# Kernel tuning notes

Measured on AMD Instinct MI355X. Metric: run time of the kernel, lower is better.

The kernel has to match this reference:

```python
import jax, jax.numpy as jnp
import numpy as np

N = 4096
D = 1024

def setup_inputs() -> dict:
    key = jax.random.key(0)
    k1, k2, k3, k4, k5, k6 = jax.random.split(key, 6)
    x_l = jax.random.normal(k1, (1, N, D), dtype=jnp.float32)
    x_r = jax.random.normal(k2, (1, N, D), dtype=jnp.float32)
    # mask encodes: (u,v) in legal_pairs AND locator[u,v] endpoints not in bucket
    mask = jax.random.randint(k3, (N, N), 0, 2) > 0
    # xavier_uniform for bilinear matrix
    limit = float(np.sqrt(6.0 / (D + D)))
    matrix = jax.random.uniform(k4, (D, D), dtype=jnp.float32, minval=-limit, maxval=limit)
    bias = jnp.zeros((1,), dtype=jnp.float32)
    wl = jax.random.normal(k5, (1, D), dtype=jnp.float32) * 0.02
    bl = jnp.zeros((1,), dtype=jnp.float32)
    wr = jax.random.normal(k6, (1, D), dtype=jnp.float32) * 0.02
    br = jnp.zeros((1,), dtype=jnp.float32)
    return {"x_l": x_l, "x_r": x_r, "mask": mask, "matrix": matrix,
            "bias": bias, "wl": wl, "bl": bl, "wr": wr, "br": br, "s_ind": 0}

def reference(x_l, x_r, mask, matrix, bias, wl, bl, wr, br, s_ind):
    # biaffine: x_l @ M @ x_r^T + bias  -> [1, n, n]
    xm = jnp.einsum('bnl,lr->bnr', x_l, matrix)
    x = jnp.einsum('bnr,bmr->bnm', xm, x_r) + bias[0]
    # linear terms: lin_l(x_l) -> [1,n,1]; lin_r(x_r)^T -> [1,1,n]
    lin_l = jnp.einsum('bnl,ol->bno', x_l, wl) + bl  # [1, n, 1]
    lin_r = jnp.einsum('bnr,or->bno', x_r, wr) + br  # [1, n, 1]
    x = x + lin_l + jnp.swapaxes(lin_r, 1, 2)
    x = jax.nn.relu(x)
    x = x[0]  # squeeze batch -> [n, n]
    # vectorized form of the legal_pairs / hypergraph-bucket scatter loop
    scores = jnp.where(mask, x, jnp.zeros((), dtype=x.dtype))
    return (scores, x)
```

## Files before the change

kernel.cpp:

```cpp
#include <hip/hip_runtime.h>
#include <stdint.h>
#include <stddef.h>

#define NTOK 4096
#define DDIM 1024

typedef __attribute__((ext_vector_type(4))) float f32x4;
typedef __attribute__((ext_vector_type(8))) short s16x8;
typedef __attribute__((ext_vector_type(4))) unsigned short u16x4;
typedef __attribute__((ext_vector_type(4))) int i32x4;

__device__ __forceinline__ unsigned short f2bf(float f) {
  union { float f; unsigned u; } v; v.f = f;
  unsigned u = v.u + 0x7fffu + ((v.u >> 16) & 1u);
  return (unsigned short)(u >> 16);
}

__device__ __forceinline__ void gload_lds16(const void* g, void* l) {
  __builtin_amdgcn_global_load_lds(
      (const __attribute__((address_space(1))) void*)g,
      (__attribute__((address_space(3))) void*)l, 16, 0, 0);
}

#define VMWAIT(N) asm volatile("s_waitcnt vmcnt(" #N ")" ::: "memory")

__global__ void convlin_k(const float* __restrict__ x, const float* __restrict__ w,
                          const float* __restrict__ b0, const float* __restrict__ b1,
                          unsigned short* __restrict__ xb, float* __restrict__ lin) {
  int wv = threadIdx.x >> 6, lane = threadIdx.x & 63;
  int row = blockIdx.x * 4 + wv;
  const f32x4* xr = (const f32x4*)(x + (size_t)row * DDIM);
  const f32x4* w4 = (const f32x4*)w;
  u16x4* xb4 = (u16x4*)(xb + (size_t)row * DDIM);
  float s = 0.f;
  for (int j = lane; j < DDIM / 4; j += 64) {
    f32x4 a = xr[j], c = w4[j];
    s += a[0] * c[0] + a[1] * c[1] + a[2] * c[2] + a[3] * c[3];
    u16x4 o;
    o[0] = f2bf(a[0]); o[1] = f2bf(a[1]); o[2] = f2bf(a[2]); o[3] = f2bf(a[3]);
    xb4[j] = o;
  }
#pragma unroll
  for (int off = 32; off; off >>= 1) s += __shfl_down(s, off);
  if (lane == 0) lin[row] = s + b0[0] + (b1 ? b1[0] : 0.f);
}

__global__ void transpose_bf16_k(const float* __restrict__ M,
                                 unsigned short* __restrict__ Mt) {
  __shared__ unsigned short tile[32][33];
  int tx = threadIdx.x, ty = threadIdx.y;
  int bx = blockIdx.x, by = blockIdx.y;
  int x = bx * 32 + tx;
  for (int i = ty; i < 32; i += 8)
    tile[i][tx] = f2bf(M[(size_t)(by * 32 + i) * DDIM + x]);
  __syncthreads();
  int ox = by * 32 + tx;
  for (int i = ty; i < 32; i += 8)
    Mt[(size_t)(bx * 32 + i) * DDIM + ox] = tile[tx][i];
}

__global__ void detect_mask_k(const unsigned char* __restrict__ m, int* __restrict__ flag) {
  __shared__ int f;
  if (threadIdx.x == 0) f = 0;
  __syncthreads();
  int any = 0;
  for (int i = threadIdx.x; i < 4096; i += 256)
    if ((i & 3) && m[i]) any = 1;
  if (any) atomicOr(&f, 1);
  __syncthreads();
  if (threadIdx.x == 0) *flag = f;
}

__launch_bounds__(512, 4)
__global__ void gemm1_k(const unsigned short* __restrict__ A,
                        const unsigned short* __restrict__ B,
                        unsigned short* __restrict__ Cb) {
  constexpr int BM = 64, BN = 128, K = DDIM;
  constexpr int MF = 2, NF = 2, AI = 1, BI = 2;
  __shared__ unsigned short As[2][BM][64];
  __shared__ unsigned short Bs[2][BN][64];

  const int lin = blockIdx.x;
  const int cpx = gridDim.x >> 3;
  const int swz = (lin & 7) * cpx + (lin >> 3);
  const int bi = swz >> 3, bj = swz & 7;

  const int tid = threadIdx.x;
  const int wid = tid >> 6, lane = tid & 63;
  const int wr2 = wid >> 2, wc2 = wid & 3;
  const int l15 = lane & 15, l16 = lane >> 4;
  const int xm = lane & 7;

  const int srow0 = tid >> 3;
  const int swslot = (tid & 7) ^ (srow0 & 7);
  const unsigned short* Ag = A + (size_t)(bi * BM + srow0) * K + swslot * 8;
  const unsigned short* Bg = B + (size_t)(bj * BN + srow0) * K + swslot * 8;

  f32x4 acc[MF][NF] = {};

#define STAGE_G1(BUF, K0)                                                    \
  {                                                                          \
    _Pragma("unroll") for (int j = 0; j < AI; ++j)                           \
        gload_lds16(Ag + (size_t)(j * 64) * K + (K0),                        \
                    &As[BUF][0][0] + j * 4096 + wid * 512);                  \
    _Pragma("unroll") for (int j = 0; j < BI; ++j)                           \
        gload_lds16(Bg + (size_t)(j * 64) * K + (K0),                        \
                    &Bs[BUF][0][0] + j * 4096 + wid * 512);                  \
  }

  STAGE_G1(0, 0)
  VMWAIT(0);
  __builtin_amdgcn_s_barrier();

  for (int t = 0; t < 16; ++t) {
    const int cur = t & 1, nxt = cur ^ 1;
    if (t < 15) STAGE_G1(nxt, (t + 1) * 64)
#pragma unroll
    for (int kk = 0; kk < 2; ++kk) {
      s16x8 Areg[MF], Breg[NF];
#pragma unroll
      for (int m = 0; m < MF; ++m)
        Areg[m] = *(const s16x8*)&As[cur][wr2 * 32 + m * 16 + l15]
                                     [(((kk << 2) | l16) ^ xm) << 3];
#pragma unroll
      for (int n = 0; n < NF; ++n)
        Breg[n] = *(const s16x8*)&Bs[cur][wc2 * 32 + n * 16 + l15]
                                     [(((kk << 2) | l16) ^ xm) << 3];
      __builtin_amdgcn_s_setprio(1);
#pragma unroll
      for (int m = 0; m < MF; ++m)
#pragma unroll
        for (int n = 0; n < NF; ++n)
          acc[m][n] = __builtin_amdgcn_mfma_f32_16x16x32_bf16(
              Areg[m], Breg[n], acc[m][n], 0, 0, 0);
      __builtin_amdgcn_s_setprio(0);
    }
    VMWAIT(0);
    __builtin_amdgcn_s_barrier();
  }
#undef STAGE_G1

#pragma unroll
  for (int m = 0; m < MF; ++m) {
    int row0 = bi * BM + wr2 * 32 + m * 16 + 4 * l16;
#pragma unroll
    for (int n = 0; n < NF; ++n) {
      int col = bj * BN + wc2 * 32 + n * 16 + l15;
#pragma unroll
      for (int r = 0; r < 4; ++r)
        Cb[(size_t)(row0 + r) * DDIM + col] = f2bf(acc[m][n][r]);
    }
  }
}

__launch_bounds__(256, 2)
__global__ void gemm2_k(const unsigned short* __restrict__ A,
                        const unsigned short* __restrict__ B,
                        const float* __restrict__ linl,
                        const float* __restrict__ linr,
                        const void* __restrict__ mask,
                        const int* __restrict__ mflag,
                        float* __restrict__ scores,
                        float* __restrict__ xout) {
  constexpr int K = DDIM;
  __shared__ __align__(16) unsigned short sAB[4 * 8192];
  unsigned short* sA = sAB;
  unsigned short* sB = sAB + 2 * 8192;

  const int lin = blockIdx.x;
  const int xcd = lin & 7, s = lin >> 3;
  const int p = (s >> 5) * 8 + xcd;
  const int w = s & 31;
  const int bi = (p >> 2) * 4 + (w >> 3);
  const int bj = (p & 3) * 8 + (w & 7);

  const int tid = threadIdx.x;
  const int wid = tid >> 6, lane = tid & 63;
  const int wr2 = wid >> 1, wc2 = wid & 1;
  const int l15 = lane & 15, l16 = lane >> 4;
  const int xm = lane & 7;

  const int srow0 = tid >> 3;
  const int swslot = (tid & 7) ^ (srow0 & 7);
  const unsigned short* Ag = A + (size_t)(bi * 128 + srow0) * K + swslot * 8;
  const unsigned short* Bg = B + (size_t)(bj * 128 + srow0) * K + swslot * 8;

  f32x4 acc[4][4] = {};

#define STG2(BUF, K0)                                                        \
  {                                                                          \
    _Pragma("unroll") for (int j = 0; j < 4; ++j) {                          \
      gload_lds16(Ag + (size_t)(j * 32) * K + (K0),                          \
                  sA + (BUF)*8192 + j * 2048 + wid * 512);                   \
      gload_lds16(Bg + (size_t)(j * 32) * K + (K0),                          \
                  sB + (BUF)*8192 + j * 2048 + wid * 512);                   \
    }                                                                        \
  }

  STG2(0, 0)
  VMWAIT(0);
  __builtin_amdgcn_s_barrier();

  for (int t = 0; t < 16; ++t) {
    const int cur = t & 1, nxt = cur ^ 1;
    if (t < 15) STG2(nxt, (t + 1) * 64)
#pragma unroll
    for (int kk = 0; kk < 2; ++kk) {
      s16x8 Areg[4], Breg[4];
#pragma unroll
      for (int m = 0; m < 4; ++m)
        Areg[m] = *(const s16x8*)(sA + cur * 8192 +
                                  (wr2 * 64 + m * 16 + l15) * 64 +
                                  ((((kk << 2) | l16) ^ xm) << 3));
#pragma unroll
      for (int n = 0; n < 4; ++n)
        Breg[n] = *(const s16x8*)(sB + cur * 8192 +
                                  (wc2 * 64 + n * 16 + l15) * 64 +
                                  ((((kk << 2) | l16) ^ xm) << 3));
      __builtin_amdgcn_s_setprio(1);
#pragma unroll
      for (int m = 0; m < 4; ++m)
#pragma unroll
        for (int n = 0; n < 4; ++n)
          acc[m][n] = __builtin_amdgcn_mfma_f32_16x16x32_bf16(
              Areg[m], Breg[n], acc[m][n], 0, 0, 0);
      __builtin_amdgcn_s_setprio(0);
    }
    VMWAIT(0);
    __builtin_amdgcn_s_barrier();
  }
#undef STG2

  __syncthreads();
  float* Cf = (float*)sAB;
#pragma unroll
  for (int m = 0; m < 4; ++m) {
#pragma unroll
    for (int n = 0; n < 4; ++n) {
      int lc = wc2 * 64 + n * 16 + l15;
#pragma unroll
      for (int r = 0; r < 4; ++r) {
        int lr = wr2 * 64 + m * 16 + l16 * 4 + r;
        Cf[lr * 128 + (lc ^ (((lr >> 2) & 1) << 4))] = acc[m][n][r];
      }
    }
  }
  __syncthreads();

  const int mf = *mflag;
#pragma unroll
  for (int it = 0; it < 16; ++it) {
    int fid = it * 256 + tid;
    int lr = fid >> 5, sl = fid & 31;
    int c0 = sl << 2;
    int cs = c0 ^ (((lr >> 2) & 1) << 4);
    f32x4 v4 = *(const f32x4*)&Cf[lr * 128 + cs];
    int row = bi * 128 + lr;
    int colb = bj * 128 + c0;
    float ll = linl[row];
    f32x4 rr = *(const f32x4*)&linr[colb];
    size_t idx = (size_t)row * NTOK + colb;
    f32x4 o, sc;
    if (mf) {
      unsigned m4 = *(const unsigned*)((const unsigned char*)mask + idx);
#pragma unroll
      for (int e = 0; e < 4; ++e) {
        float v = v4[e] + ll + rr[e];
        v = v > 0.f ? v : 0.f;
        o[e] = v; sc[e] = ((m4 >> (8 * e)) & 255u) ? v : 0.f;
      }
    } else {
      i32x4 m4 = *(const i32x4*)((const int*)mask + idx);
#pragma unroll
      for (int e = 0; e < 4; ++e) {
        float v = v4[e] + ll + rr[e];
        v = v > 0.f ? v : 0.f;
        o[e] = v; sc[e] = m4[e] ? v : 0.f;
      }
    }
    *(f32x4*)&xout[idx] = o;
    *(f32x4*)&scores[idx] = sc;
  }
}

extern "C" void kernel_launch(void* const* d_in, const int* in_sizes, int n_in,
                              void* d_out, int out_size, void* d_ws, size_t ws_size,
                              hipStream_t stream) {
  const float* x_l    = (const float*)d_in[0];
  const float* x_r    = (const float*)d_in[1];
  const void*  maskp  = (const void*)d_in[2];
  const float* matrix = (const float*)d_in[3];
  const float* bias   = (const float*)d_in[4];
  const float* wl     = (const float*)d_in[5];
  const float* bl     = (const float*)d_in[6];
  const float* wr     = (const float*)d_in[7];
  const float* br     = (const float*)d_in[8];

  unsigned short* XLb = (unsigned short*)d_ws;
  unsigned short* XRb = XLb + (size_t)NTOK * DDIM;
  unsigned short* XMb = XRb + (size_t)NTOK * DDIM;
  unsigned short* Mtb = XMb + (size_t)NTOK * DDIM;
  float* lin_l = (float*)(Mtb + (size_t)DDIM * DDIM);
  float* lin_r = lin_l + NTOK;
  int* mflag = (int*)(lin_r + NTOK);

  float* scores = (float*)d_out;
  float* xout = scores + (size_t)NTOK * NTOK;

  convlin_k<<<NTOK / 4, 256, 0, stream>>>(x_l, wl, bl, bias, XLb, lin_l);
  convlin_k<<<NTOK / 4, 256, 0, stream>>>(x_r, wr, br, nullptr, XRb, lin_r);
  transpose_bf16_k<<<dim3(32, 32), dim3(32, 8), 0, stream>>>(matrix, Mtb);
  detect_mask_k<<<1, 256, 0, stream>>>((const unsigned char*)maskp, mflag);

  gemm1_k<<<512, 512, 0, stream>>>(XLb, Mtb, XMb);

  gemm2_k<<<1024, 256, 0, stream>>>(XMb, XRb, lin_l, lin_r, maskp, mflag,
                                    scores, xout);
}
```

Measured before the change: 108.2 us.

## Restructure gemm2 to 8 waves, BK=32 tiles and half-tile epilogue staging

The second GEMM kernel goes from 256 to 512 threads per block and each wave now owns a 64x32 sub-tile. The K step shrinks from 64 to 32 with a matching smaller LDS double buffer and new swizzle. The epilogue stages the 128x128 result through LDS in two 64-row halves so it fits the smaller shared buffer. The aim is higher occupancy and more waves to hide latency, at the cost of twice as many barriers per K loop and lower MFMA work per LDS load.

New measurement: 127.5 us. +17.8%, slower.

```diff
diff --git a/kernel.cpp b/kernel.cpp
--- a/kernel.cpp
+++ b/kernel.cpp
@@ -153,7 +153,7 @@
   }
 }
 
-__launch_bounds__(256, 2)
+__launch_bounds__(512, 8)
 __global__ void gemm2_k(const unsigned short* __restrict__ A,
                         const unsigned short* __restrict__ B,
                         const float* __restrict__ linl,
@@ -163,9 +163,9 @@
                         float* __restrict__ scores,
                         float* __restrict__ xout) {
   constexpr int K = DDIM;
-  __shared__ __align__(16) unsigned short sAB[4 * 8192];
+  __shared__ __align__(16) unsigned short sAB[4 * 4096];
   unsigned short* sA = sAB;
-  unsigned short* sB = sAB + 2 * 8192;
+  unsigned short* sB = sAB + 2 * 4096;
 
   const int lin = blockIdx.x;
   const int xcd = lin & 7, s = lin >> 3;
@@ -176,52 +176,47 @@
 
   const int tid = threadIdx.x;
   const int wid = tid >> 6, lane = tid & 63;
-  const int wr2 = wid >> 1, wc2 = wid & 1;
+  const int wr2 = wid >> 2, wc2 = wid & 3;
   const int l15 = lane & 15, l16 = lane >> 4;
-  const int xm = lane & 7;
-
-  const int srow0 = tid >> 3;
-  const int swslot = (tid & 7) ^ (srow0 & 7);
+  const int xs = (l15 >> 1) & 3;
+
+  const int srow0 = tid >> 2;
+  const int swslot = (tid & 3) ^ ((srow0 >> 1) & 3);
   const unsigned short* Ag = A + (size_t)(bi * 128 + srow0) * K + swslot * 8;
   const unsigned short* Bg = B + (size_t)(bj * 128 + srow0) * K + swslot * 8;
 
-  f32x4 acc[4][4] = {};
+  f32x4 acc[4][2] = {};
 
 #define STG2(BUF, K0)                                                        \
   {                                                                          \
-    _Pragma("unroll") for (int j = 0; j < 4; ++j) {                          \
-      gload_lds16(Ag + (size_t)(j * 32) * K + (K0),                          \
-                  sA + (BUF)*8192 + j * 2048 + wid * 512);                   \
-      gload_lds16(Bg + (size_t)(j * 32) * K + (K0),                          \
-                  sB + (BUF)*8192 + j * 2048 + wid * 512);                   \
-    }                                                                        \
+    gload_lds16(Ag + (K0), sA + (BUF)*4096 + wid * 512);                     \
+    gload_lds16(Bg + (K0), sB + (BUF)*4096 + wid * 512);                     \
   }
 
   STG2(0, 0)
   VMWAIT(0);
   __builtin_amdgcn_s_barrier();
 
-  for (int t = 0; t < 16; ++t) {
+  for (int t = 0; t < 32; ++t) {
     const int cur = t & 1, nxt = cur ^ 1;
-    if (t < 15) STG2(nxt, (t + 1) * 64)
-#pragma unroll
-    for (int kk = 0; kk < 2; ++kk) {
-      s16x8 Areg[4], Breg[4];
+    if (t < 31) STG2(nxt, (t + 1) * 32)
+    {
+      const unsigned short* As0 = sA + cur * 4096;
+      const unsigned short* Bs0 = sB + cur * 4096;
+      s16x8 Areg[4], Breg[2];
 #pragma unroll
       for (int m = 0; m < 4; ++m)
-        Areg[m] = *(const s16x8*)(sA + cur * 8192 +
-                                  (wr2 * 64 + m * 16 + l15) * 64 +
-                                  ((((kk << 2) | l16) ^ xm) << 3));
-#pragma unroll
-      for (int n = 0; n < 4; ++n)
-        Breg[n] = *(const s16x8*)(sB + cur * 8192 +
-                                  (wc2 * 64 + n * 16 + l15) * 64 +
-                                  ((((kk << 2) | l16) ^ xm) << 3));
+        Areg[m] = *(const s16x8*)(As0 + (wr2 * 64 + m * 16 + l15) * 32 +
+                                  ((l16 ^ xs) << 3));
+#pragma unroll
+      for (int n = 0; n < 2; ++n)
+        Breg[n] = *(const s16x8*)(Bs0 + (wc2 * 32 + n * 16 + l15) * 32 +
+                                  ((l16 ^ xs) << 3));
       __builtin_amdgcn_s_setprio(1);
 #pragma unroll
       for (int m = 0; m < 4; ++m)
 #pragma unroll
-        for (int n = 0; n < 4; ++n)
+        for (int n = 0; n < 2; ++n)
           acc[m][n] = __builtin_amdgcn_mfma_f32_16x16x32_bf16(
               Areg[m], Breg[n], acc[m][n], 0, 0, 0);
       __builtin_amdgcn_s_setprio(0);
@@ -231,55 +226,59 @@
   }
 #undef STG2
 
-  __syncthreads();
+  const int mf = *mflag;
   float* Cf = (float*)sAB;
 #pragma unroll
-  for (int m = 0; m < 4; ++m) {
-#pragma unroll
-    for (int n = 0; n < 4; ++n) {
-      int lc = wc2 * 64 + n * 16 + l15;
-#pragma unroll
-      for (int r = 0; r < 4; ++r) {
-        int lr = wr2 * 64 + m * 16 + l16 * 4 + r;
-        Cf[lr * 128 + (lc ^ (((lr >> 2) & 1) << 4))] = acc[m][n][r];
+  for (int h = 0; h < 2; ++h) {
+    __syncthreads();
+    if (wr2 == h) {
+#pragma unroll
+      for (int m = 0; m < 4; ++m) {
+#pragma unroll
+        for (int n = 0; n < 2; ++n) {
+          int lc = wc2 * 32 + n * 16 + l15;
+#pragma unroll
+          for (int r = 0; r < 4; ++r) {
+            int lr = m * 16 + l16 * 4 + r;
+            Cf[lr * 128 + (lc ^ (((lr >> 2) & 1) << 4))] = acc[m][n][r];
+          }
+        }
       }
     }
-  }
-  __syncthreads();
-
-  const int mf = *mflag;
-#pragma unroll
-  for (int it = 0; it < 16; ++it) {
-    int fid = it * 256 + tid;
-    int lr = fid >> 5, sl = fid & 31;
-    int c0 = sl << 2;
-    int cs = c0 ^ (((lr >> 2) & 1) << 4);
-    f32x4 v4 = *(const f32x4*)&Cf[lr * 128 + cs];
-    int row = bi * 128 + lr;
-    int colb = bj * 128 + c0;
-    float ll = linl[row];
-    f32x4 rr = *(const f32x4*)&linr[colb];
-    size_t idx = (size_t)row * NTOK + colb;
-    f32x4 o, sc;
-    if (mf) {
-      unsigned m4 = *(const unsigned*)((const unsigned char*)mask + idx);
-#pragma unroll
-      for (int e = 0; e < 4; ++e) {
-        float v = v4[e] + ll + rr[e];
-        v = v > 0.f ? v : 0.f;
-        o[e] = v; sc[e] = ((m4 >> (8 * e)) & 255u) ? v : 0.f;
+    __syncthreads();
+#pragma unroll
+    for (int it = 0; it < 4; ++it) {
+      int fid = it * 512 + tid;
+      int lr = fid >> 5, sl = fid & 31;
+      int c0 = sl << 2;
+      int cs = c0 ^ (((lr >> 2) & 1) << 4);
+      f32x4 v4 = *(const f32x4*)&Cf[lr * 128 + cs];
+      int row = bi * 128 + h * 64 + lr;
+      int colb = bj * 128 + c0;
+      float ll = linl[row];
+      f32x4 rr = *(const f32x4*)&linr[colb];
+      size_t idx = (size_t)row * NTOK + colb;
+      f32x4 o, sc;
+      if (mf) {
+        unsigned m4 = *(const unsigned*)((const unsigned char*)mask + idx);
+#pragma unroll
+        for (int e = 0; e < 4; ++e) {
+          float v = v4[e] + ll + rr[e];
+          v = v > 0.f ? v : 0.f;
+          o[e] = v; sc[e] = ((m4 >> (8 * e)) & 255u) ? v : 0.f;
+        }
+      } else {
+        i32x4 m4 = *(const i32x4*)((const int*)mask + idx);
+#pragma unroll
+        for (int e = 0; e < 4; ++e) {
+          float v = v4[e] + ll + rr[e];
+          v = v > 0.f ? v : 0.f;
+          o[e] = v; sc[e] = m4[e] ? v : 0.f;
+        }
       }
-    } else {
-      i32x4 m4 = *(const i32x4*)((const int*)mask + idx);
-#pragma unroll
-      for (int e = 0; e < 4; ++e) {
-        float v = v4[e] + ll + rr[e];
-        v = v > 0.f ? v : 0.f;
-        o[e] = v; sc[e] = m4[e] ? v : 0.f;
-      }
-    }
-    *(f32x4*)&xout[idx] = o;
-    *(f32x4*)&scores[idx] = sc;
+      *(f32x4*)&xout[idx] = o;
+      *(f32x4*)&scores[idx] = sc;
+    }
   }
 }
 
@@ -314,6 +313,6 @@
 
   gemm1_k<<<512, 512, 0, stream>>>(XLb, Mtb, XMb);
 
-  gemm2_k<<<1024, 256, 0, stream>>>(XMb, XRb, lin_l, lin_r, maskp, mflag,
+  gemm2_k<<<1024, 512, 0, stream>>>(XMb, XRb, lin_l, lin_r, maskp, mflag,
                                     scores, xout);
 }
```
